# Kernel tuning notes

Hardware: AMD Instinct MI355X
Metric: run time of the kernel (lower is better)

## Reference

```python
import jax, jax.numpy as jnp
import numpy as np
import math

NH = 8      # n_heads
EPS = 1e-5  # LayerNorm eps (torch default)

def _pe(S, D):
    # Sin/cos positional encoding, faithful to PositionalEncoder
    pos = jnp.arange(S, dtype=jnp.float32)[:, None]
    div = jnp.exp(jnp.arange(0, D, 2, dtype=jnp.float32) * (-math.log(10000.0) / D))
    ang = pos * div  # (S, D/2)
    pe = jnp.zeros((S, D), jnp.float32)
    pe = pe.at[:, 0::2].set(jnp.sin(ang)).at[:, 1::2].set(jnp.cos(ang))
    return pe

def _ln(x, g, b):
    m = x.mean(-1, keepdims=True)
    v = ((x - m) ** 2).mean(-1, keepdims=True)
    return (x - m) / jnp.sqrt(v + EPS) * g + b

def setup_inputs() -> dict:
    key = jax.random.key(0)
    ks = jax.random.split(key, 6)
    S, H, W, D, dff = 512, 4, 4, 512, 2048
    x = jax.random.normal(ks[0], (S, H, W, D), jnp.float32)
    s = 1.0 / math.sqrt(D)
    Wq = jax.random.normal(ks[1], (D, D), jnp.float32) * s      # w_qs (used for q, k, v in sincos path)
    Wfc = jax.random.normal(ks[2], (D, D), jnp.float32) * s     # fc (no bias)
    W1 = jax.random.normal(ks[3], (dff, D), jnp.float32) * s    # ffn.w1
    b1 = jnp.zeros((dff,), jnp.float32)
    W2 = jax.random.normal(ks[4], (D, dff), jnp.float32) * (1.0 / math.sqrt(dff))  # ffn.w2
    b2 = jnp.zeros((D,), jnp.float32)
    g1 = jnp.ones((D,), jnp.float32); be1 = jnp.zeros((D,), jnp.float32)
    g2 = jnp.ones((D,), jnp.float32); be2 = jnp.zeros((D,), jnp.float32)
    return dict(x=x, Wq=Wq, Wfc=Wfc, W1=W1, b1=b1, W2=W2, b2=b2,
                g1=g1, be1=be1, g2=g2, be2=be2)

def reference(x, Wq, Wfc, W1, b1, W2, b2, g1, be1, g2, be2):
    S, H, Wd, D = x.shape
    depth = D // NH
    # sincos path: ALL of q,k,v use w_qs (source bug) and q==k==v since inputs are identical
    q = x @ Wq.T + _pe(S, D)[:, None, None, :]               # (S,H,W,D)
    # torch .view: raw memory reinterpretation (S,H,W,D) -> (H,W,S,NH,depth), then transpose(2,3)
    q5 = jnp.swapaxes(q.reshape(H, Wd, S, NH, depth), 2, 3)  # (H,W,NH,S,depth)
    k_t = jnp.swapaxes(q5, 3, 4)                             # (H,W,NH,depth,S)
    scale = 1.0 / math.sqrt(depth)
    # 'hwink,hwijm->hwinm': k and j are summed INDEPENDENTLY (rank-1 outer product of sums)
    bmm_qk = jnp.einsum('hwink,hwijm->hwinm', q5 * scale, k_t)   # (H,W,NH,S,S)
    qk = jax.nn.softmax(bmm_qk, axis=-1)
    qk = jnp.einsum('hwink,hwijm->hwinm', qk, k_t)               # second context pass
    attn_weights = jax.nn.softmax(qk, axis=-1)
    out = jnp.einsum('hwijk,hwikn->hwijn', attn_weights, q5)     # v == q5; (H,W,NH,S,depth)
    attn_out = out.reshape(S, H, Wd, NH * depth) @ Wfc.T         # raw reshape back, then fc
    o1 = _ln(x + attn_out, g1, be1)
    ffn = jax.nn.relu(o1 @ W1.T + b1) @ W2.T + b2
    return _ln(o1 + ffn, g2, be2)
```

## Files before the change

kernel.cpp:

```cpp
#include <hip/hip_runtime.h>
#include <hip/hip_bf16.h>
#include <math.h>


typedef short short8 __attribute__((ext_vector_type(8)));
typedef float f32x4 __attribute__((ext_vector_type(4)));

#define LN10K_OVER_256 0.03597789207803197f

__device__ __forceinline__ void gload16(const short* g, short* l) {
  __builtin_amdgcn_global_load_lds(
      (const __attribute__((address_space(1))) void*)g,
      (__attribute__((address_space(3))) void*)l, 16, 0, 0);
}

#define BAR() do { asm volatile("" ::: "memory"); \
                   __builtin_amdgcn_s_barrier();  \
                   asm volatile("" ::: "memory"); } while (0)

__device__ __forceinline__ short8 ldsfrag(const short* opbuf, int R, int fq) {
  int sr = R >> 1;
  int sp = (((R & 1) << 2) | fq) ^ (sr & 7);
  return *(const short8*)(opbuf + sr * 64 + sp * 8);
}

template<bool DOSTAGE, int WAITK>
__device__ __forceinline__ void tile_step(
    short* ldsb, int cur, int nx, int tt, int koff,
    const short* Ag0, const short* Ag1, const short* Bg0, const short* Bg1,
    int w, int fr, int fq, int wm, int wn, f32x4 (&acc)[8][4]) {
  const short* Abuf = ldsb + cur * 16384;
  const short* Bbuf = Abuf + 8192;
  short8 af[4], bfr[4];
#pragma unroll
  for (int m = 0; m < 4; ++m) af[m] = ldsfrag(Abuf, wm + m * 16 + fr, fq);
#pragma unroll
  for (int n = 0; n < 4; ++n) bfr[n] = ldsfrag(Bbuf, wn + n * 16 + fr, fq);
  if (DOSTAGE) {
    int kb = koff + (tt + 2) * 32;
    gload16(Ag0 + kb, ldsb + nx * 16384 + w * 512);
    gload16(Ag1 + kb, ldsb + nx * 16384 + 4096 + w * 512);
  }
  BAR();
  __builtin_amdgcn_s_setprio(1);
#pragma unroll
  for (int m = 0; m < 4; ++m)
#pragma unroll
    for (int n = 0; n < 4; ++n)
      acc[m][n] = __builtin_amdgcn_mfma_f32_16x16x32_bf16(af[m], bfr[n],
                                                          acc[m][n], 0, 0, 0);
  __builtin_amdgcn_s_setprio(0);
  BAR();
#pragma unroll
  for (int m = 0; m < 4; ++m) af[m] = ldsfrag(Abuf, wm + 64 + m * 16 + fr, fq);
  if (DOSTAGE) {
    int kb = koff + (tt + 2) * 32;
    gload16(Bg0 + kb, ldsb + nx * 16384 + 8192 + w * 512);
    gload16(Bg1 + kb, ldsb + nx * 16384 + 8192 + 4096 + w * 512);
  }
  BAR();
  __builtin_amdgcn_s_setprio(1);
#pragma unroll
  for (int m = 0; m < 4; ++m)
#pragma unroll
    for (int n = 0; n < 4; ++n)
      acc[4 + m][n] = __builtin_amdgcn_mfma_f32_16x16x32_bf16(af[m], bfr[n],
                                                              acc[4 + m][n], 0, 0, 0);
  __builtin_amdgcn_s_setprio(0);
  if (WAITK == 4) asm volatile("s_waitcnt vmcnt(4)" ::: "memory");
  else if (WAITK == 0) asm volatile("s_waitcnt vmcnt(0)" ::: "memory");
  BAR();
}

template<int MODE, int NT>
__global__ __launch_bounds__(512) void gemm256(
    const short* __restrict__ A, const short* __restrict__ B,
    const float* __restrict__ bias,
    short* __restrict__ C0, short* __restrict__ C1,
    short* __restrict__ C2, short* __restrict__ C3,
    int ldC, int ldA, int ldB) {
  __shared__ short lds[3 * 2 * 8192];
  const int t = threadIdx.x;
  const int w = t >> 6, l = t & 63;
  const int fr = l & 15, fq = l >> 4;
  const int wm = (w >> 2) * 128;
  const int wn = (w & 3) * 64;
  const int m0 = blockIdx.y * 256, n0 = blockIdx.x * 256;
  const int z = blockIdx.z;
  const int koff = z * (NT * 32);

  const int scont = (t & 7) ^ ((t >> 3) & 7);
  const int Rbase = ((t >> 3) << 1) | (scont >> 2);
  const int cg = (scont & 3) << 3;
  const short* Ag0 = A + (size_t)(m0 + Rbase) * ldA + cg;
  const short* Ag1 = Ag0 + (size_t)128 * ldA;
  const short* Bg0 = B + (size_t)(n0 + Rbase) * ldB + cg;
  const short* Bg1 = Bg0 + (size_t)128 * ldB;
  short* ldsb = &lds[0];

  gload16(Ag0 + koff, ldsb + w * 512);
  gload16(Ag1 + koff, ldsb + 4096 + w * 512);
  gload16(Bg0 + koff, ldsb + 8192 + w * 512);
  gload16(Bg1 + koff, ldsb + 8192 + 4096 + w * 512);
  gload16(Ag0 + koff + 32, ldsb + 16384 + w * 512);
  gload16(Ag1 + koff + 32, ldsb + 16384 + 4096 + w * 512);
  gload16(Bg0 + koff + 32, ldsb + 16384 + 8192 + w * 512);
  gload16(Bg1 + koff + 32, ldsb + 16384 + 8192 + 4096 + w * 512);
  asm volatile("s_waitcnt vmcnt(4)" ::: "memory");
  BAR();

  f32x4 acc[8][4] = {};
  int cur = 0;
#pragma unroll 1
  for (int tt = 0; tt < NT - 2; ++tt) {
    int nx = cur + 2; if (nx >= 3) nx -= 3;
    tile_step<true, 4>(ldsb, cur, nx, tt, koff, Ag0, Ag1, Bg0, Bg1,
                       w, fr, fq, wm, wn, acc);
    if (++cur == 3) cur = 0;
  }
  tile_step<false, 0>(ldsb, cur, 0, NT - 2, koff, Ag0, Ag1, Bg0, Bg1,
                      w, fr, fq, wm, wn, acc);
  { int c2 = cur + 1; if (c2 >= 3) c2 -= 3;
    tile_step<false, -1>(ldsb, c2, 0, NT - 1, koff, Ag0, Ag1, Bg0, Bg1,
                         w, fr, fq, wm, wn, acc); }

  short* myC;
  if (MODE == 1 || MODE == 0) myC = C0;
  else myC = (z == 0) ? C0 : (z == 1) ? C1 : (z == 2) ? C2 : C3;
  float bv[4];
  if (MODE == 1) {
#pragma unroll
    for (int n = 0; n < 4; ++n) bv[n] = bias[n0 + wn + n * 16 + fr];
  }
#pragma unroll
  for (int mm = 0; mm < 8; ++mm) {
    const float* per = nullptr;
    if (MODE == 0) {
      int s = (m0 + wm + mm * 16) >> 4;
      per = bias + (size_t)s * 512;
    }
#pragma unroll
    for (int n = 0; n < 4; ++n) {
      int col = n0 + wn + n * 16 + fr;
      float pv = (MODE == 0) ? per[col] : 0.f;
#pragma unroll
      for (int j = 0; j < 4; ++j) {
        int row = m0 + wm + mm * 16 + fq * 4 + j;
        float v = acc[mm][n][j];
        if (MODE == 1) v = fmaxf(v + bv[n], 0.f);
        if (MODE == 0) v += pv;
        __hip_bfloat16 hb = __float2bfloat16(v);
        myC[(size_t)row * ldC + col] = *(short*)&hb;
      }
    }
  }
}

__device__ __forceinline__ void cvt8(const float* in, short* out, int i) {
  const float4* p = (const float4*)(in + (size_t)i * 8);
  float4 a = p[0], b = p[1];
  union { __hip_bfloat16 h[8]; short8 s; } u;
  u.h[0] = __float2bfloat16(a.x); u.h[1] = __float2bfloat16(a.y);
  u.h[2] = __float2bfloat16(a.z); u.h[3] = __float2bfloat16(a.w);
  u.h[4] = __float2bfloat16(b.x); u.h[5] = __float2bfloat16(b.y);
  u.h[6] = __float2bfloat16(b.z); u.h[7] = __float2bfloat16(b.w);
  *(short8*)(out + (size_t)i * 8) = u.s;
}

__global__ __launch_bounds__(256) void prep(
    const float* __restrict__ x, const float* __restrict__ W1,
    const float* __restrict__ W2, const float* __restrict__ Wq,
    const float* __restrict__ Wfc,
    short* __restrict__ xb, short* __restrict__ W1b,
    short* __restrict__ W2b, short* __restrict__ Wqb,
    float* __restrict__ wsum, float* __restrict__ pe) {
  int b = blockIdx.x, t = threadIdx.x;
  if (b < 2048) {
    cvt8(x, xb, b * 256 + t);
  } else if (b < 2560) {
    cvt8(W1, W1b, (b - 2048) * 256 + t);
  } else if (b < 3072) {
    cvt8(W2, W2b, (b - 2560) * 256 + t);
  } else if (b < 3200) {
    cvt8(Wq, Wqb, (b - 3072) * 256 + t);
  } else if (b < 3328) {
    int idx = (b - 3200) * 256 + t;
    int n = idx >> 6, d = idx & 63;
    float s = 0.f;
#pragma unroll
    for (int j = 0; j < 8; ++j) s += Wfc[(size_t)n * 512 + j * 64 + d];
    wsum[idx] = s;
  } else {
    int idx = (b - 3328) * 256 + t;
    int s = idx >> 9, c = idx & 511;
    float f = expf(-(float)(c >> 1) * LN10K_OVER_256);
    float ang = (float)s * f;
    pe[idx] = (c & 1) ? cosf(ang) : sinf(ang);
  }
}

__global__ __launch_bounds__(256) void attn_g(
    const short* __restrict__ qb, const float* __restrict__ x,
    const float* __restrict__ wsum, const float* __restrict__ g1,
    const float* __restrict__ be1, float* __restrict__ o1,
    short* __restrict__ o1b) {
  int g = blockIdx.x;
  int hw = g >> 3, i = g & 7;
  int t = threadIdx.x;
  __shared__ short sl[512 * 72];
  __shared__ float a_[512];
  __shared__ float adist_[512];
  __shared__ float pctx[4][64];
  __shared__ float gb[1024];
  __shared__ float redA[4], redB[4], redMS[2];
  __shared__ float ctxs[64];

  gb[t] = g1[t]; gb[t + 256] = g1[t + 256];
  gb[512 + t] = be1[t]; gb[768 + t] = be1[t + 256];

  {
    const short* qsrc = qb + ((size_t)hw * 512) * 512 + i * 64;
    int chunk = t & 7, jr0 = t >> 3;
#pragma unroll
    for (int rep = 0; rep < 16; ++rep) {
      int j = jr0 + rep * 32;
      *(short8*)&sl[j * 72 + chunk * 8] =
          *(const short8*)(qsrc + (size_t)j * 512 + chunk * 8);
    }
  }
  __syncthreads();

  float r0 = 0.f, r1 = 0.f;
#pragma unroll
  for (int c = 0; c < 8; ++c) {
    union { short8 s8; short e[8]; } u0, u1;
    u0.s8 = *(const short8*)&sl[t * 72 + c * 8];
    u1.s8 = *(const short8*)&sl[(t + 256) * 72 + c * 8];
#pragma unroll
    for (int u = 0; u < 8; ++u) {
      r0 += __bfloat162float(*(__hip_bfloat16*)&u0.e[u]);
      r1 += __bfloat162float(*(__hip_bfloat16*)&u1.e[u]);
    }
  }
  float m = fmaxf(r0, r1);
  for (int off = 32; off; off >>= 1) m = fmaxf(m, __shfl_down(m, off));
  int wid = t >> 6, lane = t & 63;
  if (lane == 0) redA[wid] = m;
  __syncthreads();
  if (t == 0) redMS[0] = fmaxf(fmaxf(redA[0], redA[1]), fmaxf(redA[2], redA[3]));
  __syncthreads();
  float M = redMS[0];
  float e0 = expf(r0 - M), e1 = expf(r1 - M);
  float s = e0 + e1;
  for (int off = 32; off; off >>= 1) s += __shfl_down(s, off);
  if (lane == 0) redB[wid] = s;
  __syncthreads();
  if (t == 0) redMS[1] = redB[0] + redB[1] + redB[2] + redB[3];
  __syncthreads();
  float inv = 1.f / redMS[1];
  a_[t] = e0 * inv;
  a_[t + 256] = e1 * inv;
  __syncthreads();

  {
    int d = t & 63, seg = t >> 6;
    float acc = 0.f;
    for (int mm = seg * 128; mm < seg * 128 + 128; ++mm)
      acc += a_[mm] * __bfloat162float(*(__hip_bfloat16*)&sl[mm * 72 + d]);
    pctx[seg][d] = acc;
  }
  __syncthreads();
  if (t < 64) ctxs[t] = pctx[0][t] + pctx[1][t] + pctx[2][t] + pctx[3][t];
  __syncthreads();

  for (int n = t; n < 512; n += 256) {
    const float4* wr = (const float4*)(wsum + (size_t)n * 64);
    float sa = 0.f;
#pragma unroll
    for (int db = 0; db < 16; ++db) {
      float4 wv = wr[db];
      float4 cv = *(const float4*)&ctxs[db * 4];
      sa += cv.x * wv.x + cv.y * wv.y + cv.z * wv.z + cv.w * wv.w;
    }
    adist_[n] = sa;
  }
  __syncthreads();

  const float4* x4 = (const float4*)x;
  int w = t >> 6;
#pragma unroll 1
  for (int u = 0; u < 16; ++u) {
    int j = i * 64 + w * 16 + u;
    size_t R = (size_t)hw * 512 + j;
    float4 xv0 = x4[R * 128 + lane * 2];
    float4 xv1 = x4[R * 128 + lane * 2 + 1];
    float4 a0 = *(const float4*)&adist_[lane * 8];
    float4 a1 = *(const float4*)&adist_[lane * 8 + 4];
    float v[8] = {xv0.x + a0.x, xv0.y + a0.y, xv0.z + a0.z, xv0.w + a0.w,
                  xv1.x + a1.x, xv1.y + a1.y, xv1.z + a1.z, xv1.w + a1.w};
    float sm_ = 0.f, sq = 0.f;
#pragma unroll
    for (int q = 0; q < 8; ++q) { sm_ += v[q]; sq += v[q] * v[q]; }
    for (int off = 32; off; off >>= 1) {
      sm_ += __shfl_xor(sm_, off);
      sq += __shfl_xor(sq, off);
    }
    float mean = sm_ * (1.f / 512.f);
    float var = sq * (1.f / 512.f) - mean * mean;
    float rinv = rsqrtf(var + 1e-5f);
    float o[8];
    union { __hip_bfloat16 h[8]; short8 s8; } ub;
#pragma unroll
    for (int q = 0; q < 8; ++q) {
      int c = lane * 8 + q;
      o[q] = (v[q] - mean) * rinv * gb[c] + gb[512 + c];
      ub.h[q] = __float2bfloat16(o[q]);
    }
    float4 w0 = {o[0], o[1], o[2], o[3]};
    float4 w1 = {o[4], o[5], o[6], o[7]};
    *(float4*)&o1[R * 512 + lane * 8] = w0;
    *(float4*)&o1[R * 512 + lane * 8 + 4] = w1;
    *(short8*)&o1b[R * 512 + lane * 8] = ub.s8;
  }
}

__global__ __launch_bounds__(256) void ln2_fused(
    const float* __restrict__ o1,
    const short* __restrict__ p0, const short* __restrict__ p1,
    const short* __restrict__ p2, const short* __restrict__ p3,
    const float* __restrict__ b2, const float* __restrict__ gamma,
    const float* __restrict__ beta, float* __restrict__ Out) {
  int r = blockIdx.x;
  int t = threadIdx.x;
  size_t base = (size_t)r * 512;
  float v[2];
#pragma unroll
  for (int h = 0; h < 2; ++h) {
    int c = t + h * 256;
    float f = b2[c];
    f += __bfloat162float(*(const __hip_bfloat16*)&p0[base + c]);
    f += __bfloat162float(*(const __hip_bfloat16*)&p1[base + c]);
    f += __bfloat162float(*(const __hip_bfloat16*)&p2[base + c]);
    f += __bfloat162float(*(const __hip_bfloat16*)&p3[base + c]);
    v[h] = o1[base + c] + f;
  }
  float s = v[0] + v[1], sq = v[0] * v[0] + v[1] * v[1];
  __shared__ float red[6];
  __shared__ float redA[4];
  __shared__ float redB[4];
  for (int off = 32; off; off >>= 1) {
    s += __shfl_down(s, off);
    sq += __shfl_down(sq, off);
  }
  int wid = t >> 6, lane = t & 63;
  if (lane == 0) { redA[wid] = s; redB[wid] = sq; }
  __syncthreads();
  if (t == 0) {
    float S = redA[0] + redA[1] + redA[2] + redA[3];
    float Q = redB[0] + redB[1] + redB[2] + redB[3];
    float mean = S * (1.f / 512.f);
    float var = Q * (1.f / 512.f) - mean * mean;
    red[4] = mean;
    red[5] = rsqrtf(var + 1e-5f);
  }
  __syncthreads();
  float mean = red[4], inv = red[5];
  Out[base + t] = (v[0] - mean) * inv * gamma[t] + beta[t];
  Out[base + t + 256] = (v[1] - mean) * inv * gamma[t + 256] + beta[t + 256];
}

extern "C" void kernel_launch(void* const* d_in, const int* in_sizes, int n_in,
                              void* d_out, int out_size, void* d_ws, size_t ws_size,
                              hipStream_t stream) {
  const float* x   = (const float*)d_in[0];
  const float* Wq  = (const float*)d_in[1];
  const float* Wfc = (const float*)d_in[2];
  const float* W1  = (const float*)d_in[3];
  const float* b1  = (const float*)d_in[4];
  const float* W2  = (const float*)d_in[5];
  const float* b2  = (const float*)d_in[6];
  const float* g1  = (const float*)d_in[7];
  const float* be1 = (const float*)d_in[8];
  const float* g2  = (const float*)d_in[9];
  const float* be2 = (const float*)d_in[10];
  float* out = (float*)d_out;

  char* ws = (char*)d_ws;
  float* o1   = (float*)(ws);
  short* h1b  = (short*)(ws + (16u << 20));
  short* pz0  = (short*)(ws + (48u << 20));
  short* pz1  = (short*)(ws + (56u << 20));
  short* o1b  = (short*)(ws + (64u << 20));
  short* pz2  = (short*)(ws + (64u << 20));
  short* pz3  = (short*)(ws + (72u << 20));
  short* W1b  = (short*)(ws + (80u << 20));
  short* W2b  = (short*)(ws + (82u << 20));
  short* Wqb  = (short*)(ws + (84u << 20));
  short* xb   = (short*)(ws + (85u << 20));
  short* qb   = (short*)(ws + (93u << 20));
  float* wsum = (float*)(ws + (101u << 20));
  float* pe   = (float*)(ws + (101u << 20) + (128u << 10));

  prep<<<4352, 256, 0, stream>>>(x, W1, W2, Wq, Wfc, xb, W1b, W2b, Wqb, wsum, pe);
  gemm256<0, 16><<<dim3(2, 32, 1), 512, 0, stream>>>(
      xb, Wqb, pe, qb, qb, qb, qb, 512, 512, 512);
  attn_g<<<128, 256, 0, stream>>>(qb, x, wsum, g1, be1, o1, o1b);
  gemm256<1, 16><<<dim3(8, 32, 1), 512, 0, stream>>>(
      o1b, W1b, b1, h1b, h1b, h1b, h1b, 2048, 512, 512);
  gemm256<3, 16><<<dim3(2, 32, 4), 512, 0, stream>>>(
      h1b, W2b, nullptr, pz0, pz1, pz2, pz3, 512, 2048, 2048);
  ln2_fused<<<8192, 256, 0, stream>>>(o1, pz0, pz1, pz2, pz3, b2, g2, be2, out);
}
```

Measured before the change: 115.6 us.

## Replace split-K W2 GEMM with 128x128-tile full-K GEMM and simplify LN2

The FFN down-projection previously used 256x256 tiles with a 4-way split-K, writing four bf16 partial outputs that the LN2 kernel then summed. It now uses a new 128x128-tile GEMM (256 threads) that runs the full K=2048 loop, adds the bias in its epilogue and writes one output. The Q projection also moves to the 128-tile kernel, which gives more blocks. This removes the extra partial-sum traffic and reduces LN2 to one input, but each block now runs a longer serial K loop and the smaller tiles reuse less data.

```diff
diff --git a/kernel.cpp b/kernel.cpp
--- a/kernel.cpp
+++ b/kernel.cpp
@@ -75,9 +75,7 @@
 template<int MODE, int NT>
 __global__ __launch_bounds__(512) void gemm256(
     const short* __restrict__ A, const short* __restrict__ B,
-    const float* __restrict__ bias,
-    short* __restrict__ C0, short* __restrict__ C1,
-    short* __restrict__ C2, short* __restrict__ C3,
+    const float* __restrict__ bias, short* __restrict__ C0,
     int ldC, int ldA, int ldB) {
   __shared__ short lds[3 * 2 * 8192];
   const int t = threadIdx.x;
@@ -86,8 +84,7 @@
   const int wm = (w >> 2) * 128;
   const int wn = (w & 3) * 64;
   const int m0 = blockIdx.y * 256, n0 = blockIdx.x * 256;
-  const int z = blockIdx.z;
-  const int koff = z * (NT * 32);
+  const int koff = 0;
 
   const int scont = (t & 7) ^ ((t >> 3) & 7);
   const int Rbase = ((t >> 3) << 1) | (scont >> 2);
@@ -98,14 +95,14 @@
   const short* Bg1 = Bg0 + (size_t)128 * ldB;
   short* ldsb = &lds[0];
 
-  gload16(Ag0 + koff, ldsb + w * 512);
-  gload16(Ag1 + koff, ldsb + 4096 + w * 512);
-  gload16(Bg0 + koff, ldsb + 8192 + w * 512);
-  gload16(Bg1 + koff, ldsb + 8192 + 4096 + w * 512);
-  gload16(Ag0 + koff + 32, ldsb + 16384 + w * 512);
-  gload16(Ag1 + koff + 32, ldsb + 16384 + 4096 + w * 512);
-  gload16(Bg0 + koff + 32, ldsb + 16384 + 8192 + w * 512);
-  gload16(Bg1 + koff + 32, ldsb + 16384 + 8192 + 4096 + w * 512);
+  gload16(Ag0, ldsb + w * 512);
+  gload16(Ag1, ldsb + 4096 + w * 512);
+  gload16(Bg0, ldsb + 8192 + w * 512);
+  gload16(Bg1, ldsb + 8192 + 4096 + w * 512);
+  gload16(Ag0 + 32, ldsb + 16384 + w * 512);
+  gload16(Ag1 + 32, ldsb + 16384 + 4096 + w * 512);
+  gload16(Bg0 + 32, ldsb + 16384 + 8192 + w * 512);
+  gload16(Bg1 + 32, ldsb + 16384 + 8192 + 4096 + w * 512);
   asm volatile("s_waitcnt vmcnt(4)" ::: "memory");
   BAR();
 
@@ -124,16 +121,113 @@
     tile_step<false, -1>(ldsb, c2, 0, NT - 1, koff, Ag0, Ag1, Bg0, Bg1,
                          w, fr, fq, wm, wn, acc); }
 
-  short* myC;
-  if (MODE == 1 || MODE == 0) myC = C0;
-  else myC = (z == 0) ? C0 : (z == 1) ? C1 : (z == 2) ? C2 : C3;
   float bv[4];
-  if (MODE == 1) {
+#pragma unroll
+  for (int n = 0; n < 4; ++n) bv[n] = bias[n0 + wn + n * 16 + fr];
+#pragma unroll
+  for (int mm = 0; mm < 8; ++mm) {
+#pragma unroll
+    for (int n = 0; n < 4; ++n) {
+      int col = n0 + wn + n * 16 + fr;
+#pragma unroll
+      for (int j = 0; j < 4; ++j) {
+        int row = m0 + wm + mm * 16 + fq * 4 + j;
+        float v = fmaxf(acc[mm][n][j] + bv[n], 0.f);
+        __hip_bfloat16 hb = __float2bfloat16(v);
+        C0[(size_t)row * ldC + col] = *(short*)&hb;
+      }
+    }
+  }
+}
+
+template<bool DOSTAGE, int WAITK>
+__device__ __forceinline__ void tile_step128(
+    short* ldsb, int cur, int nx, int tt,
+    const short* Ag0, const short* Ag1, const short* Bg0, const short* Bg1,
+    int w, int fr, int fq, int wm, int wn, f32x4 (&acc)[4][4]) {
+  const short* Abuf = ldsb + cur * 8192;
+  const short* Bbuf = Abuf + 4096;
+  short8 af[4], bfr[4];
+#pragma unroll
+  for (int m = 0; m < 4; ++m) af[m] = ldsfrag(Abuf, wm + m * 16 + fr, fq);
+#pragma unroll
+  for (int n = 0; n < 4; ++n) bfr[n] = ldsfrag(Bbuf, wn + n * 16 + fr, fq);
+  if (DOSTAGE) {
+    int kb = (tt + 2) * 32;
+    gload16(Ag0 + kb, ldsb + nx * 8192 + w * 512);
+    gload16(Ag1 + kb, ldsb + nx * 8192 + 2048 + w * 512);
+    gload16(Bg0 + kb, ldsb + nx * 8192 + 4096 + w * 512);
+    gload16(Bg1 + kb, ldsb + nx * 8192 + 6144 + w * 512);
+  }
+  BAR();
+  __builtin_amdgcn_s_setprio(1);
+#pragma unroll
+  for (int m = 0; m < 4; ++m)
+#pragma unroll
+    for (int n = 0; n < 4; ++n)
+      acc[m][n] = __builtin_amdgcn_mfma_f32_16x16x32_bf16(af[m], bfr[n],
+                                                          acc[m][n], 0, 0, 0);
+  __builtin_amdgcn_s_setprio(0);
+  if (WAITK == 4) asm volatile("s_waitcnt vmcnt(4)" ::: "memory");
+  else if (WAITK == 0) asm volatile("s_waitcnt vmcnt(0)" ::: "memory");
+  BAR();
+}
+
+template<int MODE, int NT>
+__global__ __launch_bounds__(256) void gemm128(
+    const short* __restrict__ A, const short* __restrict__ B,
+    const float* __restrict__ bias, short* __restrict__ C,
+    int ldC, int ldA, int ldB) {
+  __shared__ short lds[3 * 8192];
+  const int t = threadIdx.x;
+  const int w = t >> 6, l = t & 63;
+  const int fr = l & 15, fq = l >> 4;
+  const int wm = (w >> 1) * 64;
+  const int wn = (w & 1) * 64;
+  const int m0 = blockIdx.y * 128, n0 = blockIdx.x * 128;
+
+  const int scont = (t & 7) ^ ((t >> 3) & 7);
+  const int Rbase = ((t >> 3) << 1) | (scont >> 2);
+  const int cg = (scont & 3) << 3;
+  const short* Ag0 = A + (size_t)(m0 + Rbase) * ldA + cg;
+  const short* Ag1 = Ag0 + (size_t)64 * ldA;
+  const short* Bg0 = B + (size_t)(n0 + Rbase) * ldB + cg;
+  const short* Bg1 = Bg0 + (size_t)64 * ldB;
+  short* ldsb = &lds[0];
+
+  gload16(Ag0, ldsb + w * 512);
+  gload16(Ag1, ldsb + 2048 + w * 512);
+  gload16(Bg0, ldsb + 4096 + w * 512);
+  gload16(Bg1, ldsb + 6144 + w * 512);
+  gload16(Ag0 + 32, ldsb + 8192 + w * 512);
+  gload16(Ag1 + 32, ldsb + 8192 + 2048 + w * 512);
+  gload16(Bg0 + 32, ldsb + 8192 + 4096 + w * 512);
+  gload16(Bg1 + 32, ldsb + 8192 + 6144 + w * 512);
+  asm volatile("s_waitcnt vmcnt(4)" ::: "memory");
+  BAR();
+
+  f32x4 acc[4][4] = {};
+  int cur = 0;
+#pragma unroll 1
+  for (int tt = 0; tt < NT - 2; ++tt) {
+    int nx = cur + 2; if (nx >= 3) nx -= 3;
+    tile_step128<true, 4>(ldsb, cur, nx, tt, Ag0, Ag1, Bg0, Bg1,
+                          w, fr, fq, wm, wn, acc);
+    if (++cur == 3) cur = 0;
+  }
+  tile_step128<false, 0>(ldsb, cur, 0, NT - 2, Ag0, Ag1, Bg0, Bg1,
+                         w, fr, fq, wm, wn, acc);
+  { int c2 = cur + 1; if (c2 >= 3) c2 -= 3;
+    tile_step128<false, -1>(ldsb, c2, 0, NT - 1, Ag0, Ag1, Bg0, Bg1,
+                            w, fr, fq, wm, wn, acc); }
+
+  float bv[4];
+  if (MODE == 2) {
 #pragma unroll
     for (int n = 0; n < 4; ++n) bv[n] = bias[n0 + wn + n * 16 + fr];
   }
 #pragma unroll
-  for (int mm = 0; mm < 8; ++mm) {
+  for (int mm = 0; mm < 4; ++mm) {
     const float* per = nullptr;
     if (MODE == 0) {
       int s = (m0 + wm + mm * 16) >> 4;
@@ -142,15 +236,13 @@
 #pragma unroll
     for (int n = 0; n < 4; ++n) {
       int col = n0 + wn + n * 16 + fr;
-      float pv = (MODE == 0) ? per[col] : 0.f;
+      float pv = (MODE == 0) ? per[col] : bv[n];
 #pragma unroll
       for (int j = 0; j < 4; ++j) {
         int row = m0 + wm + mm * 16 + fq * 4 + j;
-        float v = acc[mm][n][j];
-        if (MODE == 1) v = fmaxf(v + bv[n], 0.f);
-        if (MODE == 0) v += pv;
+        float v = acc[mm][n][j] + pv;
         __hip_bfloat16 hb = __float2bfloat16(v);
-        myC[(size_t)row * ldC + col] = *(short*)&hb;
+        C[(size_t)row * ldC + col] = *(short*)&hb;
       }
     }
   }
@@ -325,26 +417,17 @@
 }
 
 __global__ __launch_bounds__(256) void ln2_fused(
-    const float* __restrict__ o1,
-    const short* __restrict__ p0, const short* __restrict__ p1,
-    const short* __restrict__ p2, const short* __restrict__ p3,
-    const float* __restrict__ b2, const float* __restrict__ gamma,
-    const float* __restrict__ beta, float* __restrict__ Out) {
+    const float* __restrict__ o1, const short* __restrict__ f2,
+    const float* __restrict__ gamma, const float* __restrict__ beta,
+    float* __restrict__ Out) {
   int r = blockIdx.x;
   int t = threadIdx.x;
   size_t base = (size_t)r * 512;
-  float v[2];
-#pragma unroll
-  for (int h = 0; h < 2; ++h) {
-    int c = t + h * 256;
-    float f = b2[c];
-    f += __bfloat162float(*(const __hip_bfloat16*)&p0[base + c]);
-    f += __bfloat162float(*(const __hip_bfloat16*)&p1[base + c]);
-    f += __bfloat162float(*(const __hip_bfloat16*)&p2[base + c]);
-    f += __bfloat162float(*(const __hip_bfloat16*)&p3[base + c]);
-    v[h] = o1[base + c] + f;
-  }
-  float s = v[0] + v[1], sq = v[0] * v[0] + v[1] * v[1];
+  float v0 = o1[base + t] +
+             __bfloat162float(*(const __hip_bfloat16*)&f2[base + t]);
+  float v1 = o1[base + t + 256] +
+             __bfloat162float(*(const __hip_bfloat16*)&f2[base + t + 256]);
+  float s = v0 + v1, sq = v0 * v0 + v1 * v1;
   __shared__ float red[6];
   __shared__ float redA[4];
   __shared__ float redB[4];
@@ -365,8 +448,8 @@
   }
   __syncthreads();
   float mean = red[4], inv = red[5];
-  Out[base + t] = (v[0] - mean) * inv * gamma[t] + beta[t];
-  Out[base + t + 256] = (v[1] - mean) * inv * gamma[t + 256] + beta[t + 256];
+  Out[base + t] = (v0 - mean) * inv * gamma[t] + beta[t];
+  Out[base + t + 256] = (v1 - mean) * inv * gamma[t + 256] + beta[t + 256];
 }
 
 extern "C" void kernel_launch(void* const* d_in, const int* in_sizes, int n_in,
@@ -388,26 +471,23 @@
   char* ws = (char*)d_ws;
   float* o1   = (float*)(ws);
   short* h1b  = (short*)(ws + (16u << 20));
-  short* pz0  = (short*)(ws + (48u << 20));
-  short* pz1  = (short*)(ws + (56u << 20));
-  short* o1b  = (short*)(ws + (64u << 20));
-  short* pz2  = (short*)(ws + (64u << 20));
-  short* pz3  = (short*)(ws + (72u << 20));
-  short* W1b  = (short*)(ws + (80u << 20));
-  short* W2b  = (short*)(ws + (82u << 20));
-  short* Wqb  = (short*)(ws + (84u << 20));
-  short* xb   = (short*)(ws + (85u << 20));
-  short* qb   = (short*)(ws + (93u << 20));
-  float* wsum = (float*)(ws + (101u << 20));
-  float* pe   = (float*)(ws + (101u << 20) + (128u << 10));
+  short* f2b  = (short*)(ws + (48u << 20));
+  short* o1b  = (short*)(ws + (56u << 20));
+  short* W1b  = (short*)(ws + (64u << 20));
+  short* W2b  = (short*)(ws + (66u << 20));
+  short* Wqb  = (short*)(ws + (68u << 20));
+  short* xb   = (short*)(ws + (69u << 20));
+  short* qb   = (short*)(ws + (77u << 20));
+  float* wsum = (float*)(ws + (85u << 20));
+  float* pe   = (float*)(ws + (85u << 20) + (128u << 10));
 
   prep<<<4352, 256, 0, stream>>>(x, W1, W2, Wq, Wfc, xb, W1b, W2b, Wqb, wsum, pe);
-  gemm256<0, 16><<<dim3(2, 32, 1), 512, 0, stream>>>(
-      xb, Wqb, pe, qb, qb, qb, qb, 512, 512, 512);
+  gemm128<0, 16><<<dim3(4, 64), 256, 0, stream>>>(
+      xb, Wqb, pe, qb, 512, 512, 512);
   attn_g<<<128, 256, 0, stream>>>(qb, x, wsum, g1, be1, o1, o1b);
-  gemm256<1, 16><<<dim3(8, 32, 1), 512, 0, stream>>>(
-      o1b, W1b, b1, h1b, h1b, h1b, h1b, 2048, 512, 512);
-  gemm256<3, 16><<<dim3(2, 32, 4), 512, 0, stream>>>(
-      h1b, W2b, nullptr, pz0, pz1, pz2, pz3, 512, 2048, 2048);
-  ln2_fused<<<8192, 256, 0, stream>>>(o1, pz0, pz1, pz2, pz3, b2, g2, be2, out);
-}
+  gemm256<1, 16><<<dim3(8, 32), 512, 0, stream>>>(
+      o1b, W1b, b1, h1b, 2048, 512, 512);
+  gemm128<2, 64><<<dim3(4, 64), 256, 0, stream>>>(
+      h1b, W2b, b2, f2b, 512, 2048, 2048);
+  ln2_fused<<<8192, 256, 0, stream>>>(o1, f2b, g2, be2, out);
+}
```

New measurement: 103.1 us. 10.9% less time.
